# Kernel optimization log

Measured on AMD Instinct MI355X. Metric: run time of the kernel, lower is better.

Reference implementation:

```python
import jax, jax.numpy as jnp
import numpy as np


def _unfold(x, k):
    """x: [B, C, Hp, Wp] -> patches [B, C, H, W, k, k] (stride 1)."""
    H = x.shape[2] - k + 1
    W = x.shape[3] - k + 1
    rows = [jnp.stack([x[:, :, i:i + H, j:j + W] for j in range(k)], axis=-1)
            for i in range(k)]
    return jnp.stack(rows, axis=-2)  # [B,C,H,W,k,k]


def _gconv1x1(x, w):
    """Grouped 1x1 conv. x: [B,C,H,W], w: [g, out_g, in_g] -> [B,g,out_g,H,W]."""
    B, C, H, W = x.shape
    g, og, ig = w.shape
    xg = x.reshape(B, g, ig, H, W)
    return jnp.einsum('bgihw,goi->bgohw', xg, w)


def setup_inputs() -> dict:
    key = jax.random.key(0)
    ks = jax.random.split(key, 6)
    B, Cin, H, W = 4, 64, 96, 96
    Cout, g, k = 64, 8, 7
    og, ig = Cout // g, Cin // g
    fan_scale = (2.0 / Cout) ** 0.5  # kaiming-like scale for 1x1 conv
    return {
        'x': jax.random.normal(ks[0], (B, Cin, H, W), jnp.float32),
        'wq': jax.random.normal(ks[1], (g, og, ig), jnp.float32) * fan_scale,
        'wk': jax.random.normal(ks[2], (g, og, ig), jnp.float32) * fan_scale,
        'wv': jax.random.normal(ks[3], (g, og, ig), jnp.float32) * fan_scale,
        'h_emb': jax.random.normal(ks[4], (g, og // 2, k), jnp.float32),
        'w_emb': jax.random.normal(ks[5], (g, og // 2, k), jnp.float32),
    }


def reference(x, wq, wk, wv, h_emb, w_emb):
    B, C, H, W = x.shape
    g, og, _ = wq.shape
    k = h_emb.shape[-1]
    pad = (k - 1) // 2  # stride=1, padding=(k-1)//2 per module config
    xp = jnp.pad(x, ((0, 0), (0, 0), (pad, pad), (pad, pad)))

    q = _gconv1x1(x, wq)                                   # [B,g,og,H,W]
    k_full = _gconv1x1(xp, wk).reshape(B, C, H + 2 * pad, W + 2 * pad)
    v_full = _gconv1x1(xp, wv).reshape(B, C, H + 2 * pad, W + 2 * pad)

    k_unf = _unfold(k_full, k).reshape(B, g, og, H, W, k * k)
    v_unf = _unfold(v_full, k).reshape(B, g, og, H, W, k * k)

    # relative position embedding: top half channels vary along patch rows,
    # bottom half along patch cols -> [g, og, k*k]
    h_part = jnp.broadcast_to(h_emb[:, :, :, None], (g, og // 2, k, k))
    w_part = jnp.broadcast_to(w_emb[:, :, None, :], (g, og // 2, k, k))
    emb = jnp.concatenate([h_part, w_part], axis=1).reshape(g, og, k * k)

    logits = q[..., None] * (k_unf + emb[None, :, :, None, None, :])
    att = jax.nn.softmax(logits, axis=-1)                  # [B,g,og,H,W,k^2]
    out = jnp.einsum('bgchwk,bgchwk->bgchw', att, v_unf)
    return out.reshape(B, C, H, W)
```

## Files before the change

### kernel.cpp

```cpp
#include <hip/hip_runtime.h>


constexpr int Bc = 4, Cc = 64, Hc = 96, Wc = 96;
constexpr int G = 8, OG = 8, IG = 8, KK = 7, PAD = 3;
constexpr int TH = 32, TW = 16;
constexpr int SH = TH + KK - 1;
constexpr int SWD = TW + KK - 1;
constexpr int SW2 = 24;
constexpr int TILES_H = Hc / TH, TILES_W = Wc / TW;
constexpr int TILES = TILES_H * TILES_W;
constexpr int PLANE = Hc * Wc;
constexpr int OCB = 4;
constexpr float LOG2E = 1.4426950408889634f;

#define OC_LOOP(HALFC)                                                            \
  _Pragma("unroll 1")                                                             \
  for (int oc = 0; oc < OCB; ++oc) {                                              \
    float qv0 = 0.f, qv1 = 0.f;                                                   \
    _Pragma("unroll")                                                             \
    for (int i2 = 0; i2 < IG; ++i2) {                                             \
      const float wqi = wqg[oc * IG + i2];                                        \
      qv0 = fmaf(xc0[i2], wqi, qv0);                                              \
      qv1 = fmaf(xc1[i2], wqi, qv1);                                              \
    }                                                                             \
    qv0 *= LOG2E; qv1 *= LOG2E;                                                   \
    float qe0[KK], qe1[KK];                                                       \
    _Pragma("unroll")                                                             \
    for (int t = 0; t < KK; ++t) {                                                \
      const float e = ebase[oc * KK + t];                                         \
      qe0[t] = qv0 * e; qe1[t] = qv1 * e;                                         \
    }                                                                             \
    float s0a = 0.f, s0b = 0.f, o0a = 0.f, o0b = 0.f;                             \
    float s1a = 0.f, s1b = 0.f, o1a = 0.f, o1b = 0.f;                             \
    const float2* rp = &kvs[oc][r0][tx];                                          \
    _Pragma("unroll")                                                             \
    for (int i = 0; i < 8; ++i) {                                                 \
      float2 row[KK];                                                             \
      _Pragma("unroll")                                                           \
      for (int j = 0; j < KK; ++j) row[j] = rp[i * SW2 + j];                      \
      if (i < 7) {                                                                \
        _Pragma("unroll")                                                         \
        for (int j = 0; j < KK; ++j) {                                            \
          const float ev = __builtin_amdgcn_exp2f(                                \
              fmaf(qv0, row[j].x, (HALFC) ? qe0[j] : qe0[i]));                    \
          if (j & 1) { s0b += ev; o0b = fmaf(ev, row[j].y, o0b); }                \
          else       { s0a += ev; o0a = fmaf(ev, row[j].y, o0a); }                \
        }                                                                         \
      }                                                                           \
      if (i >= 1) {                                                               \
        _Pragma("unroll")                                                         \
        for (int j = 0; j < KK; ++j) {                                            \
          const float ev = __builtin_amdgcn_exp2f(                                \
              fmaf(qv1, row[j].x, (HALFC) ? qe1[j] : qe1[i - 1]));                \
          if (j & 1) { s1b += ev; o1b = fmaf(ev, row[j].y, o1b); }                \
          else       { s1a += ev; o1a = fmaf(ev, row[j].y, o1a); }                \
        }                                                                         \
      }                                                                           \
    }                                                                             \
    ob[oc * PLANE]      = (o0a + o0b) * __builtin_amdgcn_rcpf(s0a + s0b);         \
    ob[oc * PLANE + Wc] = (o1a + o1b) * __builtin_amdgcn_rcpf(s1a + s1b);         \
  }

__global__ __launch_bounds__(256, 4)
void sasa_kernel(const float* __restrict__ x,
                 const float* __restrict__ wq,
                 const float* __restrict__ wk,
                 const float* __restrict__ wv,
                 const float* __restrict__ h_emb,
                 const float* __restrict__ w_emb,
                 float* __restrict__ out)
{
    __shared__ float2 kvs[OCB][SH][SW2];

    const int tid = threadIdx.x;
    const int L = (blockIdx.x & 7) * (Bc * G * 2 * TILES / 8) + (blockIdx.x >> 3);
    const int tile = L % TILES;
    const int rest = L / TILES;
    const int half = rest & 1;
    const int gi   = (rest >> 1) & 7;
    const int b    = rest >> 4;
    const int th0  = (tile / TILES_W) * TH;
    const int tw0  = (tile % TILES_W) * TW;

    const float* xb  = x  + (size_t)(b * Cc + gi * IG) * PLANE;
    const float* wqg = wq + gi * OG * IG + half * OCB * IG;
    const float* wkg = wk + gi * OG * IG + half * OCB * IG;
    const float* wvg = wv + gi * OG * IG + half * OCB * IG;
    const float* ebase = (half ? w_emb : h_emb) + gi * (OG / 2) * KK;

    for (int e = tid; e < SH * SWD; e += 256) {
        const int hy = e / SWD, hx = e - hy * SWD;
        const int gy = th0 + hy - PAD;
        const int gx = tw0 + hx - PAD;
        const bool valid = ((unsigned)gy < (unsigned)Hc) && ((unsigned)gx < (unsigned)Wc);
        float xv[IG];
        #pragma unroll
        for (int i = 0; i < IG; ++i)
            xv[i] = valid ? xb[i * PLANE + gy * Wc + gx] : 0.0f;
        #pragma unroll
        for (int oc = 0; oc < OCB; ++oc) {
            float ka = 0.f, va = 0.f;
            #pragma unroll
            for (int i = 0; i < IG; ++i) {
                ka = fmaf(xv[i], wkg[oc * IG + i], ka);
                va = fmaf(xv[i], wvg[oc * IG + i], va);
            }
            kvs[oc][hy][hx] = make_float2(ka, va);
        }
    }
    __syncthreads();

    const int tx  = tid & 15;
    const int ty2 = tid >> 4;
    const int r0  = 2 * ty2;
    const int h0  = th0 + r0;
    const int wg  = tw0 + tx;

    float xc0[IG], xc1[IG];
    {
        const float* xp = xb + (size_t)h0 * Wc + wg;
        #pragma unroll
        for (int i = 0; i < IG; ++i) {
            xc0[i] = xp[i * PLANE];
            xc1[i] = xp[i * PLANE + Wc];
        }
    }

    float* ob = out + (size_t)(b * Cc + gi * OG + half * OCB) * PLANE
                    + (size_t)h0 * Wc + wg;

    if (half == 0) { OC_LOOP(0) } else { OC_LOOP(1) }
}

extern "C" void kernel_launch(void* const* d_in, const int* in_sizes, int n_in,
                              void* d_out, int out_size, void* d_ws, size_t ws_size,
                              hipStream_t stream)
{
    const float* x     = (const float*)d_in[0];
    const float* wq    = (const float*)d_in[1];
    const float* wk    = (const float*)d_in[2];
    const float* wv    = (const float*)d_in[3];
    const float* h_emb = (const float*)d_in[4];
    const float* w_emb = (const float*)d_in[5];
    float* out = (float*)d_out;

    const int nblocks = Bc * G * 2 * TILES;
    sasa_kernel<<<nblocks, 256, 0, stream>>>(x, wq, wk, wv, h_emb, w_emb, out);
}
```

Before: 28.61 us.

## Split channel groups into quarters per block and precompute q before barrier

Each block now handles 2 output channels instead of 4, which doubles the grid and halves shared memory per block, and launch bounds are raised to allow 8 blocks per CU. The q projection is computed once per channel ahead of the barrier, overlapping it with the K/V staging, and the shared-memory row stride becomes odd to change the bank mapping. The aim is higher occupancy and latency hiding. The cost is that the halo K/V computation and the x loads are repeated across twice as many blocks.

```diff
diff --git a/kernel.cpp b/kernel.cpp
--- a/kernel.cpp
+++ b/kernel.cpp
@@ -6,28 +6,22 @@
 constexpr int TH = 32, TW = 16;
 constexpr int SH = TH + KK - 1;
 constexpr int SWD = TW + KK - 1;
-constexpr int SW2 = 24;
+constexpr int SW2 = 25;
 constexpr int TILES_H = Hc / TH, TILES_W = Wc / TW;
 constexpr int TILES = TILES_H * TILES_W;
 constexpr int PLANE = Hc * Wc;
-constexpr int OCB = 4;
+constexpr int OCB = 2;
+constexpr int NB = Bc * G * 4 * TILES;
 constexpr float LOG2E = 1.4426950408889634f;
 
 #define OC_LOOP(HALFC)                                                            \
   _Pragma("unroll 1")                                                             \
   for (int oc = 0; oc < OCB; ++oc) {                                              \
-    float qv0 = 0.f, qv1 = 0.f;                                                   \
-    _Pragma("unroll")                                                             \
-    for (int i2 = 0; i2 < IG; ++i2) {                                             \
-      const float wqi = wqg[oc * IG + i2];                                        \
-      qv0 = fmaf(xc0[i2], wqi, qv0);                                              \
-      qv1 = fmaf(xc1[i2], wqi, qv1);                                              \
-    }                                                                             \
-    qv0 *= LOG2E; qv1 *= LOG2E;                                                   \
+    const float qv0 = qvs[oc][0], qv1 = qvs[oc][1];                               \
     float qe0[KK], qe1[KK];                                                       \
     _Pragma("unroll")                                                             \
     for (int t = 0; t < KK; ++t) {                                                \
-      const float e = ebase[oc * KK + t];                                         \
+      const float e = eb[oc * KK + t];                                            \
       qe0[t] = qv0 * e; qe1[t] = qv1 * e;                                         \
     }                                                                             \
     float s0a = 0.f, s0b = 0.f, o0a = 0.f, o0b = 0.f;                             \
@@ -61,7 +55,7 @@
     ob[oc * PLANE + Wc] = (o1a + o1b) * __builtin_amdgcn_rcpf(s1a + s1b);         \
   }
 
-__global__ __launch_bounds__(256, 4)
+__global__ __launch_bounds__(256, 8)
 void sasa_kernel(const float* __restrict__ x,
                  const float* __restrict__ wq,
                  const float* __restrict__ wk,
@@ -73,20 +67,36 @@
     __shared__ float2 kvs[OCB][SH][SW2];
 
     const int tid = threadIdx.x;
-    const int L = (blockIdx.x & 7) * (Bc * G * 2 * TILES / 8) + (blockIdx.x >> 3);
-    const int tile = L % TILES;
-    const int rest = L / TILES;
-    const int half = rest & 1;
-    const int gi   = (rest >> 1) & 7;
-    const int b    = rest >> 4;
-    const int th0  = (tile / TILES_W) * TH;
-    const int tw0  = (tile % TILES_W) * TW;
+    const int L = (blockIdx.x & 7) * (NB / 8) + (blockIdx.x >> 3);
+    const int tile    = L % TILES;
+    const int rest    = L / TILES;
+    const int quarter = rest & 3;
+    const int gi      = (rest >> 2) & 7;
+    const int b       = rest >> 5;
+    const int half    = quarter >> 1;
+    const int th0     = (tile / TILES_W) * TH;
+    const int tw0     = (tile % TILES_W) * TW;
 
     const float* xb  = x  + (size_t)(b * Cc + gi * IG) * PLANE;
-    const float* wqg = wq + gi * OG * IG + half * OCB * IG;
-    const float* wkg = wk + gi * OG * IG + half * OCB * IG;
-    const float* wvg = wv + gi * OG * IG + half * OCB * IG;
-    const float* ebase = (half ? w_emb : h_emb) + gi * (OG / 2) * KK;
+    const float* wqg = wq + gi * OG * IG + quarter * OCB * IG;
+    const float* wkg = wk + gi * OG * IG + quarter * OCB * IG;
+    const float* wvg = wv + gi * OG * IG + quarter * OCB * IG;
+    const float* eb  = (half ? w_emb : h_emb) + gi * (OG / 2) * KK
+                                              + (quarter & 1) * OCB * KK;
+
+    const int tx  = tid & 15;
+    const int r0  = 2 * (tid >> 4);
+    const int h0  = th0 + r0;
+    const int wg  = tw0 + tx;
+    float xc0[IG], xc1[IG];
+    {
+        const float* xp = xb + (size_t)h0 * Wc + wg;
+        #pragma unroll
+        for (int i = 0; i < IG; ++i) {
+            xc0[i] = xp[i * PLANE];
+            xc1[i] = xp[i * PLANE + Wc];
+        }
+    }
 
     for (int e = tid; e < SH * SWD; e += 256) {
         const int hy = e / SWD, hx = e - hy * SWD;
@@ -108,25 +118,23 @@
             kvs[oc][hy][hx] = make_float2(ka, va);
         }
     }
+
+    float qvs[OCB][2];
+    #pragma unroll
+    for (int oc = 0; oc < OCB; ++oc) {
+        float q0 = 0.f, q1 = 0.f;
+        #pragma unroll
+        for (int i = 0; i < IG; ++i) {
+            const float wqi = wqg[oc * IG + i];
+            q0 = fmaf(xc0[i], wqi, q0);
+            q1 = fmaf(xc1[i], wqi, q1);
+        }
+        qvs[oc][0] = q0 * LOG2E;
+        qvs[oc][1] = q1 * LOG2E;
+    }
     __syncthreads();
 
-    const int tx  = tid & 15;
-    const int ty2 = tid >> 4;
-    const int r0  = 2 * ty2;
-    const int h0  = th0 + r0;
-    const int wg  = tw0 + tx;
-
-    float xc0[IG], xc1[IG];
-    {
-        const float* xp = xb + (size_t)h0 * Wc + wg;
-        #pragma unroll
-        for (int i = 0; i < IG; ++i) {
-            xc0[i] = xp[i * PLANE];
-            xc1[i] = xp[i * PLANE + Wc];
-        }
-    }
-
-    float* ob = out + (size_t)(b * Cc + gi * OG + half * OCB) * PLANE
+    float* ob = out + (size_t)(b * Cc + gi * OG + quarter * OCB) * PLANE
                     + (size_t)h0 * Wc + wg;
 
     if (half == 0) { OC_LOOP(0) } else { OC_LOOP(1) }
@@ -144,6 +152,5 @@
     const float* w_emb = (const float*)d_in[5];
     float* out = (float*)d_out;
 
-    const int nblocks = Bc * G * 2 * TILES;
-    sasa_kernel<<<nblocks, 256, 0, stream>>>(x, wq, wk, wv, h_emb, w_emb, out);
+    sasa_kernel<<<NB, 256, 0, stream>>>(x, wq, wk, wv, h_emb, w_emb, out);
 }
```

Result: no change. 28.57 us (-0.1%).
